# Performance work log

Measured on AMD Instinct MI355X. Metric: run time of the kernel, lower is better.

The kernel has to match this reference:

```python
import jax, jax.numpy as jnp
import numpy as np

N_NODES = 100000
N_EDGES = 1600000
IN_DIM = 256
OUT_DIM = 128


def setup_inputs() -> dict:
    key = jax.random.key(0)
    k1, k2, k3, k4, k5 = jax.random.split(key, 5)
    h = jax.random.normal(k1, (N_NODES, IN_DIM), dtype=jnp.float32)
    # xavier_normal-ish scales for the two weight matrices
    W = jax.random.normal(k2, (IN_DIM, OUT_DIM), dtype=jnp.float32) * (2.0 / np.sqrt(IN_DIM + OUT_DIM))
    a = jax.random.normal(k3, (2 * OUT_DIM,), dtype=jnp.float32) * (2.0 / np.sqrt(2 * OUT_DIM + 1))
    src = jax.random.randint(k4, (N_EDGES,), 0, N_NODES, dtype=jnp.int32)
    dst = jax.random.randint(k5, (N_EDGES,), 0, N_NODES, dtype=jnp.int32)
    return {"h": h, "W": W, "a": a, "src": src, "dst": dst}


def reference(h, W, a, src, dst):
    n = h.shape[0]
    d = W.shape[1]
    z = h @ W  # [N, out_dim]
    # attn_fc([z_src || z_dst]) == z_src @ a[:d] + z_dst @ a[d:]
    el = z @ a[:d]  # [N]
    er = z @ a[d:]  # [N]
    e = jax.nn.leaky_relu(el[src] + er[dst])  # [E], torch default slope 0.01
    # per-destination (segment) softmax, numerically stable
    seg_max = jax.ops.segment_max(e, dst, num_segments=n)
    e_exp = jnp.exp(e - seg_max[dst])
    denom = jax.ops.segment_sum(e_exp, dst, num_segments=n)
    alpha = e_exp / denom[dst]  # [E]
    # weighted scatter-sum of source z into destinations
    h_out = jax.ops.segment_sum(alpha[:, None] * z[src], dst, num_segments=n)
    return h_out
```

## Files before the change

kernel.cpp:

```cpp
#include <hip/hip_runtime.h>
#include <cstdint>
#include <cstddef>

#define N_NODES 100000
#define N_EDGES 1600000
#define IN_DIM  256
#define OUT_DIM 128

#define BSHIFT 7
#define BNODES 128
#define NBUCK  782
#define BCAP   3200
#define CNTMAX 2816
#define MAXE   6
#define EPB    2048
#define PB     782
#define GB     1563

typedef __attribute__((ext_vector_type(8))) short bf16x8;
typedef __attribute__((ext_vector_type(4))) float f32x4;

__device__ __forceinline__ unsigned bf16rn(float f) {
    unsigned u = __float_as_uint(f);
    return (u + 0x7FFFu + ((u >> 16) & 1u)) >> 16;
}

__global__ __launch_bounds__(256) void setup_k(
    const float* __restrict__ W, unsigned short* __restrict__ w16s,
    int* __restrict__ bucket_cursor)
{
    int t = blockIdx.x * blockDim.x + threadIdx.x;
    if (t < NBUCK) bucket_cursor[t] = 0;
    if (t >= IN_DIM * OUT_DIM) return;
    int j  = t & 7;
    int n  = (t >> 3) & 15;
    int q  = (t >> 7) & 3;
    int c  = (t >> 9) & 7;
    int kc = t >> 12;
    int k   = kc * 32 + q * 8 + j;
    int dim = (c >> 1) * 32 + n * 2 + (c & 1);
    w16s[t] = (unsigned short)bf16rn(W[k * OUT_DIM + dim]);
}

__global__ __launch_bounds__(256) void pg_k(
    const int* __restrict__ src, const int* __restrict__ dst,
    int* __restrict__ bucket_cursor, unsigned* __restrict__ ebuf,
    const float* __restrict__ h, const unsigned short* __restrict__ w16s,
    const float* __restrict__ a,
    unsigned short* __restrict__ z16, float* __restrict__ el, float* __restrict__ er)
{
    __shared__ int hist[NBUCK];
    __shared__ int gbaseL[NBUCK];
    const int t = threadIdx.x;

    if (blockIdx.x < PB) {
        for (int i = t; i < NBUCK; i += 256) hist[i] = 0;
        __syncthreads();

        const int e0 = blockIdx.x * EPB;
        int bucks[8], ranks[8];
        unsigned pk[8];
        #pragma unroll
        for (int k = 0; k < 8; ++k) {
            int e = e0 + k * 256 + t;
            bucks[k] = -1;
            if (e < N_EDGES) {
                int s = src[e], d = dst[e];
                int b = d >> BSHIFT;
                bucks[k] = b;
                ranks[k] = atomicAdd(&hist[b], 1);
                pk[k] = ((unsigned)s << BSHIFT) | (unsigned)(d & (BNODES - 1));
            }
        }
        __syncthreads();
        for (int i = t; i < NBUCK; i += 256) {
            int hc = hist[i];
            gbaseL[i] = hc ? atomicAdd(&bucket_cursor[i], hc) : 0;
        }
        __syncthreads();
        #pragma unroll
        for (int k = 0; k < 8; ++k)
            if (bucks[k] >= 0) {
                int p = gbaseL[bucks[k]] + ranks[k];
                if (p < BCAP)
                    ebuf[(size_t)bucks[k] * BCAP + p] = pk[k];
            }
        return;
    }

    const int n0   = (blockIdx.x - PB) * 64;
    const int w    = t >> 6;
    const int lane = t & 63;
    const int q    = lane >> 4;
    const int col  = lane & 15;

    int row  = n0 + w * 16 + col;
    int lrow = (row < N_NODES) ? row : (N_NODES - 1);
    const float* hp = h + (size_t)lrow * IN_DIM + q * 8;

    f32x4 acc[8];
    #pragma unroll
    for (int c = 0; c < 8; ++c) acc[c] = (f32x4){0.f, 0.f, 0.f, 0.f};

    #pragma unroll
    for (int kc = 0; kc < 8; ++kc) {
        float4 v0 = *(const float4*)(hp + kc * 32);
        float4 v1 = *(const float4*)(hp + kc * 32 + 4);
        bf16x8 af;
        af[0] = (short)bf16rn(v0.x); af[1] = (short)bf16rn(v0.y);
        af[2] = (short)bf16rn(v0.z); af[3] = (short)bf16rn(v0.w);
        af[4] = (short)bf16rn(v1.x); af[5] = (short)bf16rn(v1.y);
        af[6] = (short)bf16rn(v1.z); af[7] = (short)bf16rn(v1.w);
        #pragma unroll
        for (int c = 0; c < 8; ++c) {
            bf16x8 bfr = *(const bf16x8*)&w16s[((((kc * 8 + c) * 4 + q) * 16) + col) * 8];
            acc[c] = __builtin_amdgcn_mfma_f32_16x16x32_bf16(af, bfr, acc[c], 0, 0, 0);
        }
    }

    float aL[8], aR[8];
    #pragma unroll
    for (int c = 0; c < 8; ++c) {
        int dim = (c >> 1) * 32 + col * 2 + (c & 1);
        aL[c] = a[dim];
        aR[c] = a[128 + dim];
    }
    #pragma unroll
    for (int r = 0; r < 4; ++r) {
        int node = n0 + w * 16 + q * 4 + r;
        float sl = 0.f, sr = 0.f;
        #pragma unroll
        for (int c = 0; c < 8; ++c) {
            sl += acc[c][r] * aL[c];
            sr += acc[c][r] * aR[c];
        }
        #pragma unroll
        for (int o = 1; o < 16; o <<= 1) {
            sl += __shfl_xor(sl, o, 64);
            sr += __shfl_xor(sr, o, 64);
        }
        if (node < N_NODES) {
            #pragma unroll
            for (int g = 0; g < 4; ++g) {
                unsigned u = bf16rn(acc[2 * g][r]) | (bf16rn(acc[2 * g + 1][r]) << 16);
                ((unsigned*)z16)[(size_t)node * 64 + g * 16 + col] = u;
            }
            if (col == 0) { el[node] = sl; er[node] = sr; }
        }
    }
}

__global__ __launch_bounds__(512) void bn_k(
    const int* __restrict__ bucket_cursor, const unsigned* __restrict__ ebuf,
    const float* __restrict__ el, const float* __restrict__ er,
    const unsigned* __restrict__ z16, float* __restrict__ out)
{
    __shared__ float erL[BNODES];
    __shared__ int   deg[BNODES];
    __shared__ int   off[BNODES];
    __shared__ int   wvSum[2];
    __shared__ float wL[BCAP];
    __shared__ int   sL[BCAP];

    const int b = blockIdx.x;
    const int t = threadIdx.x;
    int cnt = bucket_cursor[b];
    if (cnt > CNTMAX) cnt = CNTMAX;
    const unsigned* eb = ebuf + (size_t)b * BCAP;

    if (t < BNODES) {
        deg[t] = 0;
        int n = b * BNODES + t;
        erL[t] = (n < N_NODES) ? er[n] : 0.f;
    }
    __syncthreads();

    unsigned pv[MAXE]; int rk[MAXE]; float wv_[MAXE];
    #pragma unroll
    for (int k = 0; k < MAXE; ++k) {
        int i = t + k * 512;
        if (i < cnt) {
            unsigned v = eb[i];
            int s  = (int)(v >> BSHIFT);
            int ld = (int)(v & (BNODES - 1));
            float e = el[s] + erL[ld];
            e = (e > 0.0f) ? e : 0.01f * e;
            wv_[k] = __expf(e);
            rk[k]  = atomicAdd(&deg[ld], 1);
            pv[k]  = v;
        }
    }
    __syncthreads();

    int d = 0, pd = 0, incl = 0;
    if (t < BNODES) {
        d  = deg[t];
        pd = (d + 3) & ~3;
        incl = pd;
    }
    if (t < BNODES) {
        #pragma unroll
        for (int o = 1; o < 64; o <<= 1) {
            int x = __shfl_up(incl, o, 64);
            if ((t & 63) >= o) incl += x;
        }
        if ((t & 63) == 63) wvSum[t >> 6] = incl;
    }
    __syncthreads();
    if (t < BNODES) off[t] = ((t >= 64) ? wvSum[0] : 0) + incl - pd;
    __syncthreads();

    #pragma unroll
    for (int k = 0; k < MAXE; ++k) {
        int i = t + k * 512;
        if (i < cnt) {
            int ld = (int)(pv[k] & (BNODES - 1));
            int p  = off[ld] + rk[k];
            wL[p] = wv_[k];
            sL[p] = (int)(pv[k] >> BSHIFT);
        }
    }
    if (t < BNODES) {
        int o = off[t];
        for (int j = o + d; j < o + pd; ++j) { wL[j] = 0.0f; sL[j] = 0; }
    }
    __syncthreads();

    const int wv   = t >> 6;
    const int lane = t & 63;
    #pragma unroll 1
    for (int k = 0; k < BNODES / 8; ++k) {
        int ln = wv * (BNODES / 8) + k;
        int n  = b * BNODES + ln;
        if (n >= N_NODES) continue;
        int o   = off[ln];
        int dl  = deg[ln];
        int pdl = (dl + 3) & ~3;
        float acc0 = 0.f, acc1 = 0.f, dsum = 0.f;
        #pragma unroll 2
        for (int i = o; i < o + pdl; i += 4) {
            float w0 = wL[i],     w1 = wL[i + 1];
            float w2 = wL[i + 2], w3 = wL[i + 3];
            int   s0 = sL[i],     s1 = sL[i + 1];
            int   s2 = sL[i + 2], s3 = sL[i + 3];
            unsigned q0 = z16[(size_t)s0 * 64 + lane];
            unsigned q1 = z16[(size_t)s1 * 64 + lane];
            unsigned q2 = z16[(size_t)s2 * 64 + lane];
            unsigned q3 = z16[(size_t)s3 * 64 + lane];
            acc0 += w0 * __uint_as_float(q0 << 16)
                  + w1 * __uint_as_float(q1 << 16)
                  + w2 * __uint_as_float(q2 << 16)
                  + w3 * __uint_as_float(q3 << 16);
            acc1 += w0 * __uint_as_float(q0 & 0xFFFF0000u)
                  + w1 * __uint_as_float(q1 & 0xFFFF0000u)
                  + w2 * __uint_as_float(q2 & 0xFFFF0000u)
                  + w3 * __uint_as_float(q3 & 0xFFFF0000u);
            dsum += w0 + w1 + w2 + w3;
        }
        if (pdl > 0) {
            float inv = 1.0f / dsum;
            acc0 *= inv; acc1 *= inv;
        }
        *(float2*)&out[(size_t)n * OUT_DIM + lane * 2] = make_float2(acc0, acc1);
    }
}

extern "C" void kernel_launch(void* const* d_in, const int* in_sizes, int n_in,
                              void* d_out, int out_size, void* d_ws, size_t ws_size,
                              hipStream_t stream)
{
    (void)in_sizes; (void)n_in; (void)out_size; (void)ws_size;
    const float* h = (const float*)d_in[0];
    const float* W = (const float*)d_in[1];
    const float* a = (const float*)d_in[2];
    const int* src = (const int*)d_in[3];
    const int* dst = (const int*)d_in[4];
    float* out = (float*)d_out;

    char* ws = (char*)d_ws;
    size_t off = 0;
    auto alloc = [&](size_t bytes) -> char* {
        char* p = ws + off;
        off += (bytes + 255) & ~(size_t)255;
        return p;
    };
    unsigned short* z16  = (unsigned short*)alloc((size_t)N_NODES * OUT_DIM * 2);
    unsigned short* w16s = (unsigned short*)alloc((size_t)IN_DIM * OUT_DIM * 2);
    float*    el        = (float*)   alloc((size_t)N_NODES * 4);
    float*    er        = (float*)   alloc((size_t)N_NODES * 4);
    int*      bucket_cursor = (int*) alloc((size_t)NBUCK * 4);
    unsigned* ebuf      = (unsigned*)alloc((size_t)NBUCK * BCAP * 4);

    setup_k<<<(IN_DIM * OUT_DIM + 255) / 256, 256, 0, stream>>>(W, w16s, bucket_cursor);
    pg_k<<<PB + GB, 256, 0, stream>>>(src, dst, bucket_cursor, ebuf,
                                      h, w16s, a, z16, el, er);
    bn_k<<<NBUCK, 512, 0, stream>>>(bucket_cursor, ebuf, el, er,
                                    (const unsigned*)z16, out);
}
```

Before: 295.5 us.

## Interleave partition and GEMM blocks, prefetch h rows, pack weight+src in LDS

The combined partition/GEMM kernel now interleaves its two block types (every third block partitions edges, the others compute z), so bandwidth-heavy scatter and MFMA work run at the same time rather than in two phases. The GEMM path loads all of a row's h values into registers before the MFMA loop and adds an occupancy hint in launch bounds. The aggregation kernel packs each edge's exp-weight and source index into one 64-bit LDS entry, halving LDS reads per edge. The trade-offs are higher register pressure from the prefetch and one extra GEMM block, whose rows are clamped and which appears harmless.

```diff
diff --git a/kernel.cpp b/kernel.cpp
--- a/kernel.cpp
+++ b/kernel.cpp
@@ -15,7 +15,7 @@
 #define MAXE   6
 #define EPB    2048
 #define PB     782
-#define GB     1563
+#define GBP    1564
 
 typedef __attribute__((ext_vector_type(8))) short bf16x8;
 typedef __attribute__((ext_vector_type(4))) float f32x4;
@@ -42,7 +42,7 @@
     w16s[t] = (unsigned short)bf16rn(W[k * OUT_DIM + dim]);
 }
 
-__global__ __launch_bounds__(256) void pg_k(
+__global__ __launch_bounds__(256, 3) void pg_k(
     const int* __restrict__ src, const int* __restrict__ dst,
     int* __restrict__ bucket_cursor, unsigned* __restrict__ ebuf,
     const float* __restrict__ h, const unsigned short* __restrict__ w16s,
@@ -51,13 +51,15 @@
 {
     __shared__ int hist[NBUCK];
     __shared__ int gbaseL[NBUCK];
-    const int t = threadIdx.x;
-
-    if (blockIdx.x < PB) {
+    const int t   = threadIdx.x;
+    const int bid = blockIdx.x;
+
+    if ((bid % 3) == 2) {
+        const int pid = bid / 3;
         for (int i = t; i < NBUCK; i += 256) hist[i] = 0;
         __syncthreads();
 
-        const int e0 = blockIdx.x * EPB;
+        const int e0 = pid * EPB;
         int bucks[8], ranks[8];
         unsigned pk[8];
         #pragma unroll
@@ -88,7 +90,8 @@
         return;
     }
 
-    const int n0   = (blockIdx.x - PB) * 64;
+    const int gid  = (bid / 3) * 2 + (bid % 3);
+    const int n0   = gid * 64;
     const int w    = t >> 6;
     const int lane = t & 63;
     const int q    = lane >> 4;
@@ -98,14 +101,21 @@
     int lrow = (row < N_NODES) ? row : (N_NODES - 1);
     const float* hp = h + (size_t)lrow * IN_DIM + q * 8;
 
+    float4 va[16];
+    #pragma unroll
+    for (int kc = 0; kc < 8; ++kc) {
+        va[2 * kc]     = *(const float4*)(hp + kc * 32);
+        va[2 * kc + 1] = *(const float4*)(hp + kc * 32 + 4);
+    }
+
     f32x4 acc[8];
     #pragma unroll
     for (int c = 0; c < 8; ++c) acc[c] = (f32x4){0.f, 0.f, 0.f, 0.f};
 
     #pragma unroll
     for (int kc = 0; kc < 8; ++kc) {
-        float4 v0 = *(const float4*)(hp + kc * 32);
-        float4 v1 = *(const float4*)(hp + kc * 32 + 4);
+        float4 v0 = va[2 * kc];
+        float4 v1 = va[2 * kc + 1];
         bf16x8 af;
         af[0] = (short)bf16rn(v0.x); af[1] = (short)bf16rn(v0.y);
         af[2] = (short)bf16rn(v0.z); af[3] = (short)bf16rn(v0.w);
@@ -159,8 +169,7 @@
     __shared__ int   deg[BNODES];
     __shared__ int   off[BNODES];
     __shared__ int   wvSum[2];
-    __shared__ float wL[BCAP];
-    __shared__ int   sL[BCAP];
+    __shared__ unsigned long long wsL[BCAP];
 
     const int b = blockIdx.x;
     const int t = threadIdx.x;
@@ -197,8 +206,6 @@
         d  = deg[t];
         pd = (d + 3) & ~3;
         incl = pd;
-    }
-    if (t < BNODES) {
         #pragma unroll
         for (int o = 1; o < 64; o <<= 1) {
             int x = __shfl_up(incl, o, 64);
@@ -216,13 +223,13 @@
         if (i < cnt) {
             int ld = (int)(pv[k] & (BNODES - 1));
             int p  = off[ld] + rk[k];
-            wL[p] = wv_[k];
-            sL[p] = (int)(pv[k] >> BSHIFT);
+            wsL[p] = ((unsigned long long)__float_as_uint(wv_[k]) << 32)
+                   | (pv[k] >> BSHIFT);
         }
     }
     if (t < BNODES) {
         int o = off[t];
-        for (int j = o + d; j < o + pd; ++j) { wL[j] = 0.0f; sL[j] = 0; }
+        for (int j = o + d; j < o + pd; ++j) wsL[j] = 0ull;
     }
     __syncthreads();
 
@@ -239,14 +246,16 @@
         float acc0 = 0.f, acc1 = 0.f, dsum = 0.f;
         #pragma unroll 2
         for (int i = o; i < o + pdl; i += 4) {
-            float w0 = wL[i],     w1 = wL[i + 1];
-            float w2 = wL[i + 2], w3 = wL[i + 3];
-            int   s0 = sL[i],     s1 = sL[i + 1];
-            int   s2 = sL[i + 2], s3 = sL[i + 3];
-            unsigned q0 = z16[(size_t)s0 * 64 + lane];
-            unsigned q1 = z16[(size_t)s1 * 64 + lane];
-            unsigned q2 = z16[(size_t)s2 * 64 + lane];
-            unsigned q3 = z16[(size_t)s3 * 64 + lane];
+            unsigned long long e0 = wsL[i],     e1 = wsL[i + 1];
+            unsigned long long e2 = wsL[i + 2], e3 = wsL[i + 3];
+            float w0 = __uint_as_float((unsigned)(e0 >> 32));
+            float w1 = __uint_as_float((unsigned)(e1 >> 32));
+            float w2 = __uint_as_float((unsigned)(e2 >> 32));
+            float w3 = __uint_as_float((unsigned)(e3 >> 32));
+            unsigned q0 = z16[(size_t)(unsigned)e0 * 64 + lane];
+            unsigned q1 = z16[(size_t)(unsigned)e1 * 64 + lane];
+            unsigned q2 = z16[(size_t)(unsigned)e2 * 64 + lane];
+            unsigned q3 = z16[(size_t)(unsigned)e3 * 64 + lane];
             acc0 += w0 * __uint_as_float(q0 << 16)
                   + w1 * __uint_as_float(q1 << 16)
                   + w2 * __uint_as_float(q2 << 16)
@@ -292,8 +301,8 @@
     unsigned* ebuf      = (unsigned*)alloc((size_t)NBUCK * BCAP * 4);
 
     setup_k<<<(IN_DIM * OUT_DIM + 255) / 256, 256, 0, stream>>>(W, w16s, bucket_cursor);
-    pg_k<<<PB + GB, 256, 0, stream>>>(src, dst, bucket_cursor, ebuf,
-                                      h, w16s, a, z16, el, er);
+    pg_k<<<PB + GBP, 256, 0, stream>>>(src, dst, bucket_cursor, ebuf,
+                                       h, w16s, a, z16, el, er);
     bn_k<<<NBUCK, 512, 0, stream>>>(bucket_cursor, ebuf, el, er,
                                     (const unsigned*)z16, out);
 }
```

New measurement: 288.1 us. 1.03x faster.
